# Kernel tuning notes

Measured on AMD Instinct MI355X. Metric: run time of the kernel, lower is better.

Reference implementation:

```python
import jax, jax.numpy as jnp
import numpy as np

SIZE = 512
LANG_NUM = 8
B, S, D = 32, 2048, SIZE


def setup_inputs() -> dict:
    key = jax.random.key(0)
    ks = jax.random.split(key, 10)
    sc = 1.0 / np.sqrt(D)
    inp = {
        "old_x": jax.random.normal(ks[0], (B, S, D), jnp.float32),
        "x": jax.random.normal(ks[1], (B, S, D), jnp.float32),
        "lang": jax.random.randint(ks[2], (B,), 0, LANG_NUM, jnp.int32),
        # shared linear (no bias): y = x @ W.T
        "share_W": jax.random.uniform(ks[3], (D, D), jnp.float32, -sc, sc),
        # per-language expert linears (no bias)
        "langs_W": jax.random.uniform(ks[4], (LANG_NUM, D, D), jnp.float32, -sc, sc),
        # per-language gate: layer1 (D->D with bias), layer2 (D->1 with bias)
        "gate_W1": jax.random.uniform(ks[5], (LANG_NUM, D, D), jnp.float32, -sc, sc),
        "gate_b1": jax.random.uniform(ks[6], (LANG_NUM, D), jnp.float32, -sc, sc),
        "gate_W2": jax.random.uniform(ks[7], (LANG_NUM, D), jnp.float32, -sc, sc),
        "gate_b2": jax.random.uniform(ks[8], (LANG_NUM,), jnp.float32, -sc, sc),
    }
    return inp


def reference(old_x, x, lang, share_W, langs_W, gate_W1, gate_b1, gate_W2, gate_b2):
    # shared path: [B,S,D] @ [D,D].T
    share_h = jnp.einsum("bsd,ed->bse", x, share_W)
    # gather per-sample expert weights by lang index
    Wl = langs_W[lang]            # [B,D,D]
    W1 = gate_W1[lang]            # [B,D,D]
    b1 = gate_b1[lang]            # [B,D]
    W2 = gate_W2[lang]            # [B,D]
    b2 = gate_b2[lang]            # [B]
    langs_h = jnp.einsum("bsd,bed->bse", x, Wl)
    # GateLayer on old_x: relu(L1(x)) + x -> L2 -> sigmoid
    h = jax.nn.relu(jnp.einsum("bsd,bed->bse", old_x, W1) + b1[:, None, :]) + old_x
    gate_logit = jnp.einsum("bsd,bd->bs", h, W2) + b2[:, None]
    gate_prob = jax.nn.sigmoid(gate_logit)[:, :, None]   # [B,S,1]
    return share_h * (1.0 - gate_prob) + langs_h * gate_prob
```

## Files before the change

### kernel.cpp

```cpp
#include <hip/hip_runtime.h>
#include <hip/hip_bf16.h>

#define B_ 32
#define S_ 2048
#define D_ 512

#define WS_GATE  0
#define WS_FLAG  262144
#define WS_SW    266240
#define WS_LW    (WS_SW + 64 * 8192)
#define WS_W1    (WS_LW + 512 * 8192)
#define WS_B1F   (WS_W1 + 512 * 8192)
#define WS_W2F   (WS_B1F + 16384)
#define WS_B2F   (WS_W2F + 16384)

typedef __attribute__((ext_vector_type(8))) short bf16x8;
typedef __attribute__((ext_vector_type(4))) float f32x4;
typedef unsigned short ushort_t;

__device__ __forceinline__ float b2f(ushort_t u) {
  union { unsigned int i; float f; } v; v.i = ((unsigned int)u) << 16; return v.f;
}
__device__ __forceinline__ ushort_t f2b(float f) {
  union { float f; unsigned int i; } v; v.f = f;
  return (ushort_t)((v.i + 0x7FFFu + ((v.i >> 16) & 1u)) >> 16);
}

__device__ __forceinline__ f32x4 mfma16(bf16x8 a, bf16x8 b, f32x4 c) {
  return __builtin_amdgcn_mfma_f32_16x16x32_bf16(a, b, c, 0, 0, 0);
}

__device__ __forceinline__ void gload16(const void* g, void* l) {
  __builtin_amdgcn_global_load_lds(
      (const __attribute__((address_space(1))) unsigned int*)g,
      (__attribute__((address_space(3))) unsigned int*)l, 16, 0, 0);
}

__global__ void detect_kernel(const unsigned int* __restrict__ w, int* __restrict__ flag) {
  __shared__ int cnt;
  if (threadIdx.x == 0) cnt = 0;
  __syncthreads();
  int c = 0;
  #pragma unroll
  for (int i = 0; i < 4; ++i) {
    unsigned int v = w[threadIdx.x + i * 256];
    unsigned int e = (v >> 7) & 0xFFu;
    if (e >= 110u && e <= 140u) ++c;
  }
  atomicAdd(&cnt, c);
  __syncthreads();
  if (threadIdx.x == 0) flag[0] = (cnt > 512) ? 1 : 0;
}

__device__ __forceinline__ bf16x8 read_frag(const ushort_t* tile, int row, int quad) {
  int g = quad ^ ((row >> 1) & 3);
  return *(const bf16x8*)(tile + row * 32 + g * 8);
}

template <int DT> struct TR16 { float4 f[4]; bf16x8 h[2]; };

template <int DT>
__device__ __forceinline__ void t16_load(const void* gv, size_t base, int tid, TR16<DT>& t) {
  const int row = tid >> 1, half = tid & 1;
  const size_t off = base + (size_t)row * D_ + half * 16;
  if constexpr (DT == 0) {
    const float4* s = (const float4*)((const float*)gv + off);
    t.f[0] = s[0]; t.f[1] = s[1]; t.f[2] = s[2]; t.f[3] = s[3];
  } else {
    const bf16x8* s = (const bf16x8*)((const ushort_t*)gv + off);
    t.h[0] = s[0]; t.h[1] = s[1];
  }
}
template <int DT>
__device__ __forceinline__ void t16_store(ushort_t* tile, int tid, const TR16<DT>& t) {
  const int row = tid >> 1, half = tid & 1;
  bf16x8 ch0, ch1;
  if constexpr (DT == 0) {
    ushort_t u[16];
    u[0]  = f2b(t.f[0].x); u[1]  = f2b(t.f[0].y); u[2]  = f2b(t.f[0].z); u[3]  = f2b(t.f[0].w);
    u[4]  = f2b(t.f[1].x); u[5]  = f2b(t.f[1].y); u[6]  = f2b(t.f[1].z); u[7]  = f2b(t.f[1].w);
    u[8]  = f2b(t.f[2].x); u[9]  = f2b(t.f[2].y); u[10] = f2b(t.f[2].z); u[11] = f2b(t.f[2].w);
    u[12] = f2b(t.f[3].x); u[13] = f2b(t.f[3].y); u[14] = f2b(t.f[3].z); u[15] = f2b(t.f[3].w);
    ch0 = *(const bf16x8*)u; ch1 = *(const bf16x8*)(u + 8);
  } else { ch0 = t.h[0]; ch1 = t.h[1]; }
  const int swz = (row >> 1) & 3, c0 = half * 2;
  *(bf16x8*)(tile + row * 32 + (((c0    ) ^ swz) << 3)) = ch0;
  *(bf16x8*)(tile + row * 32 + (((c0 + 1) ^ swz) << 3)) = ch1;
}

template <int DT> struct TRA { float4 f[2]; bf16x8 h; };

template <int DT>
__device__ __forceinline__ void ta_load(const void* gv, size_t base, int tid, TRA<DT>& t) {
  const int row = tid >> 2, g = tid & 3;
  const size_t off = base + (size_t)row * D_ + g * 8;
  if constexpr (DT == 0) {
    const float4* s = (const float4*)((const float*)gv + off);
    t.f[0] = s[0]; t.f[1] = s[1];
  } else {
    t.h = *(const bf16x8*)((const ushort_t*)gv + off);
  }
}
template <int DT>
__device__ __forceinline__ void ta_store(ushort_t* tile, int tid, const TRA<DT>& t) {
  const int row = tid >> 2, g = tid & 3;
  bf16x8 ch;
  if constexpr (DT == 0) {
    ushort_t u[8];
    u[0] = f2b(t.f[0].x); u[1] = f2b(t.f[0].y); u[2] = f2b(t.f[0].z); u[3] = f2b(t.f[0].w);
    u[4] = f2b(t.f[1].x); u[5] = f2b(t.f[1].y); u[6] = f2b(t.f[1].z); u[7] = f2b(t.f[1].w);
    ch = *(const bf16x8*)u;
  } else ch = t.h;
  const int swz = (row >> 1) & 3;
  *(bf16x8*)(tile + row * 32 + ((g ^ swz) << 3)) = ch;
}

__global__ __launch_bounds__(256)
void convert_kernel(const void* __restrict__ shareW, const void* __restrict__ langsW,
                    const void* __restrict__ gW1, const void* __restrict__ gb1,
                    const void* __restrict__ gW2, const void* __restrict__ gb2,
                    const int* __restrict__ flag, char* __restrict__ ws) {
  const int t = blockIdx.x, tid = threadIdx.x;
  const int dt = flag[0];
  if (t < 1088) {
    const void* src; ushort_t* dst; size_t sb;
    if (t < 64) {
      src = shareW; dst = (ushort_t*)(ws + WS_SW) + (size_t)t * 4096;
      sb = ((size_t)(t >> 4) * 128) * D_ + (size_t)(t & 15) * 32;
    } else if (t < 576) {
      const int t2 = t - 64;
      src = langsW; dst = (ushort_t*)(ws + WS_LW) + (size_t)t2 * 4096;
      sb = ((size_t)(t2 >> 6) * 512 + (size_t)((t2 >> 4) & 3) * 128) * D_ + (size_t)(t2 & 15) * 32;
    } else {
      const int t3 = t - 576;
      src = gW1; dst = (ushort_t*)(ws + WS_W1) + (size_t)t3 * 4096;
      sb = ((size_t)(t3 >> 6) * 512 + (size_t)((t3 >> 4) & 3) * 128) * D_ + (size_t)(t3 & 15) * 32;
    }
    if (dt == 0) { TR16<0> r; t16_load<0>(src, sb, tid, r); t16_store<0>(dst, tid, r); }
    else         { TR16<1> r; t16_load<1>(src, sb, tid, r); t16_store<1>(dst, tid, r); }
  } else {
    float* b1f = (float*)(ws + WS_B1F);
    float* w2f = (float*)(ws + WS_W2F);
    float* b2w = (float*)(ws + WS_B2F);
    for (int i = tid; i < 4096; i += 256) {
      b1f[i] = dt ? b2f(((const ushort_t*)gb1)[i]) : ((const float*)gb1)[i];
      w2f[i] = dt ? b2f(((const ushort_t*)gW2)[i]) : ((const float*)gW2)[i];
    }
    if (tid < 8)
      b2w[tid] = dt ? b2f(((const ushort_t*)gb2)[tid]) : ((const float*)gb2)[tid];
  }
}

struct GateSmem {
  alignas(16) ushort_t As[2][128 * 32];
  alignas(16) ushort_t Bs[2][512 * 32];
  float b1s[512], w2s[512], logit[128];
};
struct OutSmem {
  alignas(16) ushort_t As[2][128 * 32];
  alignas(16) ushort_t Ss[2][128 * 32];
  alignas(16) ushort_t Ls[2][128 * 32];
};

template <int DT>
__device__ __forceinline__ void gate_body(const void* __restrict__ old_x,
    const int* __restrict__ lang, const ushort_t* __restrict__ w1t,
    const float* __restrict__ b1f, const float* __restrict__ w2f,
    const float* __restrict__ b2w, float* __restrict__ gate, GateSmem& sm) {
  int bid = blockIdx.y * gridDim.x + blockIdx.x;
  int swz = (bid & 7) * 64 + (bid >> 3);
  const int s0 = (swz & 15) * 128;
  const int b  = swz >> 4;
  const int tid  = threadIdx.x;
  const int wave = tid >> 6, lane = tid & 63, quad = lane >> 4, ln = lane & 15;
  const int m_off = (wave >> 2) * 64;
  const int n_off = (wave & 3) * 128;
  const int lg = lang[b];

  sm.b1s[tid] = b1f[lg * 512 + tid];
  sm.w2s[tid] = w2f[lg * 512 + tid];
  if (tid < 128) sm.logit[tid] = 0.f;

  const size_t Aoff = ((size_t)b * S_ + s0) * D_;
  const ushort_t* w1base = w1t + (size_t)lg * 64 * 4096;

  auto stageB = [&](int kt, int buf) {
    #pragma unroll
    for (int c = 0; c < 4; ++c) {
      const int sl = c * 8 + wave;
      const int et = sl >> 3;
      const char* g = (const char*)(w1base + ((size_t)(et * 16 + kt)) * 4096)
                      + (sl & 7) * 1024 + lane * 16;
      gload16(g, (char*)sm.Bs[buf] + sl * 1024);
    }
  };

  f32x4 acc[4][8];
  #pragma unroll
  for (int i = 0; i < 4; ++i)
    #pragma unroll
    for (int j = 0; j < 8; ++j) { f32x4 z = {0.f, 0.f, 0.f, 0.f}; acc[i][j] = z; }

  TRA<DT> ta;
  stageB(0, 0);
  ta_load<DT>(old_x, Aoff, tid, ta);
  ta_store<DT>(sm.As[0], tid, ta);
  __syncthreads();

  const int rrow  = tid >> 2, rg = tid & 3;
  const int rslot = (rg ^ ((rrow >> 1) & 3)) << 3;
  float res = 0.f;

  for (int step = 0; step < 16; ++step) {
    const int cur = step & 1;
    if (step < 15) {
      stageB(step + 1, cur ^ 1);
      ta_load<DT>(old_x, Aoff + (step + 1) * 32, tid, ta);
    }
    bf16x8 af[4];
    #pragma unroll
    for (int mf = 0; mf < 4; ++mf)
      af[mf] = read_frag(sm.As[cur], m_off + mf * 16 + ln, quad);
    {
      bf16x8 rv = *(const bf16x8*)(sm.As[cur] + rrow * 32 + rslot);
      #pragma unroll
      for (int j = 0; j < 8; ++j)
        res += b2f((ushort_t)rv[j]) * sm.w2s[step * 32 + rg * 8 + j];
    }
    #pragma unroll
    for (int nh = 0; nh < 2; ++nh) {
      bf16x8 bfr[4];
      #pragma unroll
      for (int nf = 0; nf < 4; ++nf)
        bfr[nf] = read_frag(sm.Bs[cur], n_off + (nh * 4 + nf) * 16 + ln, quad);
      #pragma unroll
      for (int mf = 0; mf < 4; ++mf)
        #pragma unroll
        for (int nf = 0; nf < 4; ++nf)
          acc[mf][nh * 4 + nf] = mfma16(af[mf], bfr[nf], acc[mf][nh * 4 + nf]);
    }
    if (step < 15) ta_store<DT>(sm.As[cur ^ 1], tid, ta);
    __syncthreads();
  }
  atomicAdd(&sm.logit[rrow], res);

  float logacc[16];
  #pragma unroll
  for (int i = 0; i < 16; ++i) logacc[i] = 0.f;
  #pragma unroll
  for (int nf = 0; nf < 8; ++nf) {
    int e = n_off + nf * 16 + ln;
    float b1v = sm.b1s[e], w2v = sm.w2s[e];
    #pragma unroll
    for (int mf = 0; mf < 4; ++mf)
      #pragma unroll
      for (int r = 0; r < 4; ++r) {
        float v = acc[mf][nf][r] + b1v;
        logacc[mf * 4 + r] += fmaxf(v, 0.f) * w2v;
      }
  }
  #pragma unroll
  for (int off = 1; off < 16; off <<= 1)
    #pragma unroll
    for (int i = 0; i < 16; ++i)
      logacc[i] += __shfl_xor(logacc[i], off, 64);
  if (ln == 0) {
    #pragma unroll
    for (int mf = 0; mf < 4; ++mf)
      #pragma unroll
      for (int r = 0; r < 4; ++r)
        atomicAdd(&sm.logit[m_off + mf * 16 + quad * 4 + r], logacc[mf * 4 + r]);
  }
  __syncthreads();
  if (tid < 128) {
    float l = sm.logit[tid] + b2w[lg];
    gate[(size_t)b * S_ + s0 + tid] = 1.f / (1.f + expf(-l));
  }
}

__global__ __launch_bounds__(512, 2)
void gate_kernel(const void* __restrict__ old_x, const int* __restrict__ lang,
                 const ushort_t* __restrict__ w1t, const float* __restrict__ b1f,
                 const float* __restrict__ w2f, const float* __restrict__ b2w,
                 const int* __restrict__ flag, float* __restrict__ gate) {
  __shared__ GateSmem sm;
  if (flag[0] == 0) gate_body<0>(old_x, lang, w1t, b1f, w2f, b2w, gate, sm);
  else              gate_body<1>(old_x, lang, w1t, b1f, w2f, b2w, gate, sm);
}

template <int DT>
__device__ __forceinline__ void out_body(const void* __restrict__ x,
    const int* __restrict__ lang, const ushort_t* __restrict__ sWt,
    const ushort_t* __restrict__ lWt, const float* __restrict__ gate,
    void* __restrict__ out, OutSmem& sm) {
  int bid = (blockIdx.z * gridDim.y + blockIdx.y) * gridDim.x + blockIdx.x;
  int swz = (bid & 7) * 256 + (bid >> 3);
  const int eb = swz & 3, e0 = eb * 128;
  const int s0 = ((swz >> 2) & 15) * 128;
  const int b  = swz >> 6;
  const int tid  = threadIdx.x;
  const int wave = tid >> 6, lane = tid & 63, quad = lane >> 4, ln = lane & 15;
  const int m_off = (wave >> 1) * 64, n_off = (wave & 1) * 64;
  const int lg = lang[b];

  const size_t Aoff = ((size_t)b * S_ + s0) * D_;
  const ushort_t* Sbase = sWt + (size_t)eb * 16 * 4096;
  const ushort_t* Lbase = lWt + ((size_t)(lg * 4 + eb)) * 16 * 4096;

  auto stageSL = [&](int kt, int buf) {
    #pragma unroll
    for (int c = 0; c < 2; ++c) {
      const int sl = c * 4 + wave;
      const int boff = sl * 1024 + lane * 16;
      gload16((const char*)(Sbase + (size_t)kt * 4096) + boff,
              (char*)sm.Ss[buf] + sl * 1024);
      gload16((const char*)(Lbase + (size_t)kt * 4096) + boff,
              (char*)sm.Ls[buf] + sl * 1024);
    }
  };

  f32x4 accS[4][4], accL[4][4];
  #pragma unroll
  for (int i = 0; i < 4; ++i)
    #pragma unroll
    for (int j = 0; j < 4; ++j) {
      f32x4 z = {0.f, 0.f, 0.f, 0.f};
      accS[i][j] = z; accL[i][j] = z;
    }

  TR16<DT> ta;
  stageSL(0, 0);
  t16_load<DT>(x, Aoff, tid, ta);
  t16_store<DT>(sm.As[0], tid, ta);
  __syncthreads();

  for (int step = 0; step < 16; ++step) {
    const int cur = step & 1;
    if (step < 15) {
      stageSL(step + 1, cur ^ 1);
      t16_load<DT>(x, Aoff + (step + 1) * 32, tid, ta);
    }
    bf16x8 af[4], sf[4], lf[4];
    #pragma unroll
    for (int mf = 0; mf < 4; ++mf)
      af[mf] = read_frag(sm.As[cur], m_off + mf * 16 + ln, quad);
    #pragma unroll
    for (int nf = 0; nf < 4; ++nf) {
      sf[nf] = read_frag(sm.Ss[cur], n_off + nf * 16 + ln, quad);
      lf[nf] = read_frag(sm.Ls[cur], n_off + nf * 16 + ln, quad);
    }
    #pragma unroll
    for (int mf = 0; mf < 4; ++mf)
      #pragma unroll
      for (int nf = 0; nf < 4; ++nf) {
        accS[mf][nf] = mfma16(af[mf], sf[nf], accS[mf][nf]);
        accL[mf][nf] = mfma16(af[mf], lf[nf], accL[mf][nf]);
      }
    if (step < 15) t16_store<DT>(sm.As[cur ^ 1], tid, ta);
    __syncthreads();
  }

  #pragma unroll
  for (int mf = 0; mf < 4; ++mf) {
    int srow = s0 + m_off + mf * 16 + quad * 4;
    float gv[4];
    #pragma unroll
    for (int r = 0; r < 4; ++r) gv[r] = gate[(size_t)b * S_ + srow + r];
    #pragma unroll
    for (int nf = 0; nf < 4; ++nf) {
      int col = e0 + n_off + nf * 16 + ln;
      f32x4 cs = accS[mf][nf], cl = accL[mf][nf];
      #pragma unroll
      for (int r = 0; r < 4; ++r) {
        float v = cs[r] + gv[r] * (cl[r] - cs[r]);
        size_t idx = ((size_t)b * S_ + srow + r) * D_ + col;
        if constexpr (DT == 0) ((float*)out)[idx] = v;
        else                   ((ushort_t*)out)[idx] = f2b(v);
      }
    }
  }
}

__global__ __launch_bounds__(256, 2)
void out_kernel(const void* __restrict__ x, const int* __restrict__ lang,
                const ushort_t* __restrict__ sWt, const ushort_t* __restrict__ lWt,
                const float* __restrict__ gate, const int* __restrict__ flag,
                void* __restrict__ out) {
  __shared__ OutSmem sm;
  if (flag[0] == 0) out_body<0>(x, lang, sWt, lWt, gate, out, sm);
  else              out_body<1>(x, lang, sWt, lWt, gate, out, sm);
}

extern "C" void kernel_launch(void* const* d_in, const int* in_sizes, int n_in,
                              void* d_out, int out_size, void* d_ws, size_t ws_size,
                              hipStream_t stream) {
  const void* old_x  = d_in[0];
  const void* x      = d_in[1];
  const int*  lang   = (const int*)d_in[2];
  const void* shareW = d_in[3];
  const void* langsW = d_in[4];
  const void* gW1    = d_in[5];
  const void* gb1    = d_in[6];
  const void* gW2    = d_in[7];
  const void* gb2    = d_in[8];

  char*  ws   = (char*)d_ws;
  float* gate = (float*)(ws + WS_GATE);
  int*   flag = (int*)(ws + WS_FLAG);
  const ushort_t* sWt = (const ushort_t*)(ws + WS_SW);
  const ushort_t* lWt = (const ushort_t*)(ws + WS_LW);
  const ushort_t* w1t = (const ushort_t*)(ws + WS_W1);
  const float*    b1f = (const float*)(ws + WS_B1F);
  const float*    w2f = (const float*)(ws + WS_W2F);
  const float*    b2w = (const float*)(ws + WS_B2F);

  detect_kernel<<<1, 256, 0, stream>>>((const unsigned int*)old_x, flag);

  convert_kernel<<<1089, 256, 0, stream>>>(shareW, langsW, gW1, gb1, gW2, gb2,
                                           flag, ws);

  dim3 g1(S_ / 128, B_);
  gate_kernel<<<g1, dim3(512), 0, stream>>>(old_x, lang, w1t, b1f, w2f, b2w,
                                            flag, gate);

  dim3 g2(D_ / 128, S_ / 128, B_);
  out_kernel<<<g2, dim3(256), 0, stream>>>(x, lang, sWt, lWt, gate, flag, d_out);
}
```

Measured before the change: 448.4 us.

## Pre-convert activations to bf16 and use triple-buffered async-load GEMM kernels

Adds a pass that converts x and old_x from fp32 to bf16 in workspace, so the gate and output GEMM kernels can stream bf16 A tiles with direct global-to-LDS loads. The GEMMs move to three-stage LDS buffering with explicit vmcnt waits. The intent is to cut conversion work and load latency inside the main kernels. The cost is an extra full read and write of both activation tensors and a large workspace, and the new path only runs when the workspace is big enough.

```diff
diff --git a/kernel.cpp b/kernel.cpp
--- a/kernel.cpp
+++ b/kernel.cpp
@@ -13,6 +13,9 @@
 #define WS_B1F   (WS_W1 + 512 * 8192)
 #define WS_W2F   (WS_B1F + 16384)
 #define WS_B2F   (WS_W2F + 16384)
+#define WS_XB    (WS_B2F + 4096)
+#define WS_OXB   (WS_XB + 67108864LL)
+#define WS_NEED  (WS_OXB + 67108864LL)
 
 typedef __attribute__((ext_vector_type(8))) short bf16x8;
 typedef __attribute__((ext_vector_type(4))) float f32x4;
@@ -151,6 +154,261 @@
   }
 }
 
+__global__ __launch_bounds__(256)
+void xconv_kernel(const void* __restrict__ x, const void* __restrict__ oldx,
+                  const int* __restrict__ flag, ushort_t* __restrict__ xb,
+                  ushort_t* __restrict__ oxb) {
+  if (flag[0] != 0) return;
+  const long long N = (long long)B_ * S_ * D_ / 8;
+  long long i = (long long)blockIdx.x * 256 + threadIdx.x;
+  const long long stride = (long long)gridDim.x * 256;
+  for (; i < 2 * N; i += stride) {
+    const float4* s; ushort_t* d;
+    if (i < N) { s = (const float4*)x    + i * 2;       d = xb  + i * 8; }
+    else       { s = (const float4*)oldx + (i - N) * 2; d = oxb + (i - N) * 8; }
+    float4 a = s[0], b = s[1];
+    ushort_t u[8];
+    u[0] = f2b(a.x); u[1] = f2b(a.y); u[2] = f2b(a.z); u[3] = f2b(a.w);
+    u[4] = f2b(b.x); u[5] = f2b(b.y); u[6] = f2b(b.z); u[7] = f2b(b.w);
+    *(bf16x8*)d = *(const bf16x8*)u;
+  }
+}
+
+struct GateSmemA {
+  alignas(16) ushort_t As[3][128 * 32];
+  alignas(16) ushort_t Bs[3][512 * 32];
+  float b1s[512], w2s[512], logit[128];
+};
+struct OutSmemA {
+  alignas(16) ushort_t As[3][128 * 32];
+  alignas(16) ushort_t Ss[3][128 * 32];
+  alignas(16) ushort_t Ls[3][128 * 32];
+};
+
+__global__ __launch_bounds__(512, 2)
+void gate_kernel_a(const void* __restrict__ old_x, const ushort_t* __restrict__ oxb,
+                   const int* __restrict__ lang, const ushort_t* __restrict__ w1t,
+                   const float* __restrict__ b1f, const float* __restrict__ w2f,
+                   const float* __restrict__ b2w, const int* __restrict__ flag,
+                   float* __restrict__ gate) {
+  __shared__ GateSmemA sm;
+  int bid = blockIdx.y * gridDim.x + blockIdx.x;
+  int swz = (bid & 7) * 64 + (bid >> 3);
+  const int s0 = (swz & 15) * 128;
+  const int b  = swz >> 4;
+  const int tid  = threadIdx.x;
+  const int wave = tid >> 6, lane = tid & 63, quad = lane >> 4, ln = lane & 15;
+  const int m_off = (wave >> 2) * 64;
+  const int n_off = (wave & 3) * 128;
+  const int lg = lang[b];
+  const ushort_t* Abase = flag[0] ? (const ushort_t*)old_x : oxb;
+
+  sm.b1s[tid] = b1f[lg * 512 + tid];
+  sm.w2s[tid] = w2f[lg * 512 + tid];
+  if (tid < 128) sm.logit[tid] = 0.f;
+  __syncthreads();
+
+  const int arow = wave * 16 + (lane >> 2);
+  const int achk = (lane & 3) ^ ((arow >> 1) & 3);
+  const ushort_t* asrc = Abase + ((size_t)(b * S_ + s0 + arow)) * D_ + achk * 8;
+
+  const ushort_t* w1base = w1t + (size_t)lg * 64 * 4096;
+
+  auto issue = [&](int kt, int buf) {
+    gload16(asrc + (size_t)kt * 32, (char*)sm.As[buf] + wave * 1024);
+    #pragma unroll
+    for (int c = 0; c < 4; ++c) {
+      const int sl = c * 8 + wave, et = sl >> 3;
+      gload16((const char*)(w1base + ((size_t)(et * 16 + kt)) * 4096)
+                  + (sl & 7) * 1024 + lane * 16,
+              (char*)sm.Bs[buf] + sl * 1024);
+    }
+  };
+
+  f32x4 acc[4][8];
+  #pragma unroll
+  for (int i = 0; i < 4; ++i)
+    #pragma unroll
+    for (int j = 0; j < 8; ++j) { f32x4 z = {0.f, 0.f, 0.f, 0.f}; acc[i][j] = z; }
+
+  issue(0, 0); issue(1, 1);
+
+  const int rrow  = tid >> 2, rg = tid & 3;
+  const int rslot = (rg ^ ((rrow >> 1) & 3)) << 3;
+  float res = 0.f;
+
+  #pragma unroll
+  for (int t = 0; t < 16; ++t) {
+    if (t < 15) asm volatile("s_waitcnt vmcnt(5)" ::: "memory");
+    else        asm volatile("s_waitcnt vmcnt(0)" ::: "memory");
+    __builtin_amdgcn_s_barrier();
+    if (t + 2 < 16) issue(t + 2, (t + 2) % 3);
+    const ushort_t* Ab = sm.As[t % 3];
+    const ushort_t* Bb = sm.Bs[t % 3];
+    bf16x8 af[4];
+    #pragma unroll
+    for (int mf = 0; mf < 4; ++mf)
+      af[mf] = read_frag(Ab, m_off + mf * 16 + ln, quad);
+    {
+      bf16x8 rv = *(const bf16x8*)(Ab + rrow * 32 + rslot);
+      #pragma unroll
+      for (int j = 0; j < 8; ++j)
+        res += b2f((ushort_t)rv[j]) * sm.w2s[t * 32 + rg * 8 + j];
+    }
+    #pragma unroll
+    for (int nh = 0; nh < 2; ++nh) {
+      bf16x8 bfr[4];
+      #pragma unroll
+      for (int nf = 0; nf < 4; ++nf)
+        bfr[nf] = read_frag(Bb, n_off + (nh * 4 + nf) * 16 + ln, quad);
+      #pragma unroll
+      for (int mf = 0; mf < 4; ++mf)
+        #pragma unroll
+        for (int nf = 0; nf < 4; ++nf)
+          acc[mf][nh * 4 + nf] = mfma16(af[mf], bfr[nf], acc[mf][nh * 4 + nf]);
+    }
+  }
+  atomicAdd(&sm.logit[rrow], res);
+
+  float logacc[16];
+  #pragma unroll
+  for (int i = 0; i < 16; ++i) logacc[i] = 0.f;
+  #pragma unroll
+  for (int nf = 0; nf < 8; ++nf) {
+    int e = n_off + nf * 16 + ln;
+    float b1v = sm.b1s[e], w2v = sm.w2s[e];
+    #pragma unroll
+    for (int mf = 0; mf < 4; ++mf)
+      #pragma unroll
+      for (int r = 0; r < 4; ++r) {
+        float v = acc[mf][nf][r] + b1v;
+        logacc[mf * 4 + r] += fmaxf(v, 0.f) * w2v;
+      }
+  }
+  #pragma unroll
+  for (int off = 1; off < 16; off <<= 1)
+    #pragma unroll
+    for (int i = 0; i < 16; ++i)
+      logacc[i] += __shfl_xor(logacc[i], off, 64);
+  if (ln == 0) {
+    #pragma unroll
+    for (int mf = 0; mf < 4; ++mf)
+      #pragma unroll
+      for (int r = 0; r < 4; ++r)
+        atomicAdd(&sm.logit[m_off + mf * 16 + quad * 4 + r], logacc[mf * 4 + r]);
+  }
+  __syncthreads();
+  if (tid < 128) {
+    float l = sm.logit[tid] + b2w[lg];
+    gate[(size_t)b * S_ + s0 + tid] = 1.f / (1.f + expf(-l));
+  }
+}
+
+__global__ __launch_bounds__(256, 2)
+void out_kernel_a(const void* __restrict__ x, const ushort_t* __restrict__ xb,
+                  const int* __restrict__ lang, const ushort_t* __restrict__ sWt,
+                  const ushort_t* __restrict__ lWt, const float* __restrict__ gate,
+                  const int* __restrict__ flag, void* __restrict__ out) {
+  __shared__ OutSmemA sm;
+  int bid = (blockIdx.z * gridDim.y + blockIdx.y) * gridDim.x + blockIdx.x;
+  int swz = (bid & 7) * 256 + (bid >> 3);
+  const int eb = swz & 3, e0 = eb * 128;
+  const int s0 = ((swz >> 2) & 15) * 128;
+  const int b  = swz >> 6;
+  const int tid  = threadIdx.x;
+  const int wave = tid >> 6, lane = tid & 63, quad = lane >> 4, ln = lane & 15;
+  const int m_off = (wave >> 1) * 64, n_off = (wave & 1) * 64;
+  const int lg = lang[b];
+  const int dt = flag[0];
+  const ushort_t* Abase = dt ? (const ushort_t*)x : xb;
+
+  const ushort_t* Sbase = sWt + (size_t)eb * 16 * 4096;
+  const ushort_t* Lbase = lWt + ((size_t)(lg * 4 + eb)) * 16 * 4096;
+
+  const ushort_t* asrc[2];
+  #pragma unroll
+  for (int c = 0; c < 2; ++c) {
+    const int sl = c * 4 + wave;
+    const int arow = sl * 16 + (lane >> 2);
+    const int achk = (lane & 3) ^ ((arow >> 1) & 3);
+    asrc[c] = Abase + ((size_t)(b * S_ + s0 + arow)) * D_ + achk * 8;
+  }
+
+  auto issue = [&](int kt, int buf) {
+    #pragma unroll
+    for (int c = 0; c < 2; ++c) {
+      const int sl = c * 4 + wave;
+      gload16(asrc[c] + (size_t)kt * 32, (char*)sm.As[buf] + sl * 1024);
+    }
+    #pragma unroll
+    for (int c = 0; c < 2; ++c) {
+      const int sl = c * 4 + wave;
+      const int boff = sl * 1024 + lane * 16;
+      gload16((const char*)(Sbase + (size_t)kt * 4096) + boff,
+              (char*)sm.Ss[buf] + sl * 1024);
+      gload16((const char*)(Lbase + (size_t)kt * 4096) + boff,
+              (char*)sm.Ls[buf] + sl * 1024);
+    }
+  };
+
+  f32x4 accS[4][4], accL[4][4];
+  #pragma unroll
+  for (int i = 0; i < 4; ++i)
+    #pragma unroll
+    for (int j = 0; j < 4; ++j) {
+      f32x4 z = {0.f, 0.f, 0.f, 0.f};
+      accS[i][j] = z; accL[i][j] = z;
+    }
+
+  issue(0, 0); issue(1, 1);
+
+  #pragma unroll
+  for (int t = 0; t < 16; ++t) {
+    if (t < 15) asm volatile("s_waitcnt vmcnt(6)" ::: "memory");
+    else        asm volatile("s_waitcnt vmcnt(0)" ::: "memory");
+    __builtin_amdgcn_s_barrier();
+    if (t + 2 < 16) issue(t + 2, (t + 2) % 3);
+    const ushort_t* Ab = sm.As[t % 3];
+    const ushort_t* Sb = sm.Ss[t % 3];
+    const ushort_t* Lb = sm.Ls[t % 3];
+    bf16x8 af[4], sf[4], lf[4];
+    #pragma unroll
+    for (int mf = 0; mf < 4; ++mf)
+      af[mf] = read_frag(Ab, m_off + mf * 16 + ln, quad);
+    #pragma unroll
+    for (int nf = 0; nf < 4; ++nf) {
+      sf[nf] = read_frag(Sb, n_off + nf * 16 + ln, quad);
+      lf[nf] = read_frag(Lb, n_off + nf * 16 + ln, quad);
+    }
+    #pragma unroll
+    for (int mf = 0; mf < 4; ++mf)
+      #pragma unroll
+      for (int nf = 0; nf < 4; ++nf) {
+        accS[mf][nf] = mfma16(af[mf], sf[nf], accS[mf][nf]);
+        accL[mf][nf] = mfma16(af[mf], lf[nf], accL[mf][nf]);
+      }
+  }
+
+  #pragma unroll
+  for (int mf = 0; mf < 4; ++mf) {
+    int srow = s0 + m_off + mf * 16 + quad * 4;
+    float4 gv = *(const float4*)&gate[(size_t)b * S_ + srow];
+    #pragma unroll
+    for (int nf = 0; nf < 4; ++nf) {
+      int col = e0 + n_off + nf * 16 + ln;
+      f32x4 cs = accS[mf][nf], cl = accL[mf][nf];
+      float gr[4] = {gv.x, gv.y, gv.z, gv.w};
+      #pragma unroll
+      for (int r = 0; r < 4; ++r) {
+        float v = cs[r] + gr[r] * (cl[r] - cs[r]);
+        size_t idx = ((size_t)b * S_ + srow + r) * D_ + col;
+        if (dt == 0) ((float*)out)[idx] = v;
+        else         ((ushort_t*)out)[idx] = f2b(v);
+      }
+    }
+  }
+}
+
 struct GateSmem {
   alignas(16) ushort_t As[2][128 * 32];
   alignas(16) ushort_t Bs[2][512 * 32];
@@ -413,16 +671,26 @@
   const float*    b1f = (const float*)(ws + WS_B1F);
   const float*    w2f = (const float*)(ws + WS_W2F);
   const float*    b2w = (const float*)(ws + WS_B2F);
+  ushort_t* xb  = (ushort_t*)(ws + WS_XB);
+  ushort_t* oxb = (ushort_t*)(ws + WS_OXB);
+
+  const bool tierA = ws_size >= (size_t)WS_NEED;
 
   detect_kernel<<<1, 256, 0, stream>>>((const unsigned int*)old_x, flag);
-
   convert_kernel<<<1089, 256, 0, stream>>>(shareW, langsW, gW1, gb1, gW2, gb2,
                                            flag, ws);
 
   dim3 g1(S_ / 128, B_);
-  gate_kernel<<<g1, dim3(512), 0, stream>>>(old_x, lang, w1t, b1f, w2f, b2w,
-                                            flag, gate);
-
   dim3 g2(D_ / 128, S_ / 128, B_);
-  out_kernel<<<g2, dim3(256), 0, stream>>>(x, lang, sWt, lWt, gate, flag, d_out);
-}
+  if (tierA) {
+    xconv_kernel<<<3072, 256, 0, stream>>>(x, old_x, flag, xb, oxb);
+    gate_kernel_a<<<g1, dim3(512), 0, stream>>>(old_x, oxb, lang, w1t, b1f, w2f,
+                                                b2w, flag, gate);
+    out_kernel_a<<<g2, dim3(256), 0, stream>>>(x, xb, lang, sWt, lWt, gate,
+                                               flag, d_out);
+  } else {
+    gate_kernel<<<g1, dim3(512), 0, stream>>>(old_x, lang, w1t, b1f, w2f, b2w,
+                                              flag, gate);
+    out_kernel<<<g2, dim3(256), 0, stream>>>(x, lang, sWt, lWt, gate, flag, d_out);
+  }
+}
```

Measured after the change: 495.3 us. +10.5%, slower.
